# Performance work log

Measured on AMD Instinct MI355X. Metric: run time of the kernel, lower is better.

Reference implementation:

```python
import jax, jax.numpy as jnp
import numpy as np


def setup_inputs() -> dict:
    key = jax.random.key(0)
    kq, kk, kv = jax.random.split(key, 3)
    B, T, D = 8, 4096, 64
    q = jax.random.normal(kq, (B, T, D), dtype=jnp.float32)
    k = jax.random.normal(kk, (B, T, D), dtype=jnp.float32)
    v = jax.random.normal(kv, (B, T, D), dtype=jnp.float32)
    return {"q": q, "k": k, "v": v}


def reference(q, k, v):
    # q,k,v: [b, t, d]
    b, t_q, d = q.shape
    t_k = k.shape[1]
    scale = 1.0 / jnp.sqrt(jnp.asarray(d, dtype=q.dtype))
    qk = jnp.einsum('bqd,bkd->bqk', q, k) * scale  # [b, t_q, t_k]
    # causal mask: positions t2 > t1 set to -inf (replaces the Python double-loop)
    causal_mask = jnp.arange(t_k)[None, :] > jnp.arange(t_q)[:, None]  # [t_q, t_k]
    qk = jnp.where(causal_mask[None, :, :], -jnp.inf, qk)
    attn = jax.nn.softmax(qk, axis=-1)
    return jnp.einsum('bqk,bkd->bqd', attn, v)
```

## Files before the change

### kernel.cpp

```cpp
#include <hip/hip_runtime.h>

namespace {

constexpr float QSC = 0.18033688f;

typedef short bf16x8 __attribute__((ext_vector_type(8)));
typedef float f32x4 __attribute__((ext_vector_type(4)));

typedef __attribute__((address_space(3))) unsigned int lds_u32;
typedef __attribute__((address_space(1))) const unsigned int gbl_u32;

__device__ inline float exp2x(float x) { return __builtin_amdgcn_exp2f(x); }

__device__ inline unsigned int pack2(float a, float b) {
  unsigned int ua = __builtin_bit_cast(unsigned int, a);
  unsigned int ub = __builtin_bit_cast(unsigned int, b);
  ua = (ua + 0x8000u) >> 16;
  ub = (ub + 0x8000u) & 0xFFFF0000u;
  return ua | ub;
}

__device__ inline void gl_lds16(const unsigned short* g, unsigned short* l) {
  __builtin_amdgcn_global_load_lds((gbl_u32*)g, (lds_u32*)l, 16, 0, 0);
}

__device__ inline bf16x8 ld16(const unsigned short* p) {
  uint4 u = *(const uint4*)p;
  return __builtin_bit_cast(bf16x8, u);
}

__global__ __launch_bounds__(256) void prep(const float* __restrict__ K,
                                            const float* __restrict__ V,
                                            unsigned short* __restrict__ Kbf,
                                            unsigned short* __restrict__ Vtb) {
  __shared__ float Vl[64 * 65];
  const int bid = blockIdx.x;
  const int b = bid >> 6, kt = bid & 63;
  const int tid = threadIdx.x;
  const float4* Ks4 = (const float4*)(K + ((size_t)b * 4096 + kt * 64) * 64);
  const float4* Vs4 = (const float4*)(V + ((size_t)b * 4096 + kt * 64) * 64);
  #pragma unroll
  for (int i = 0; i < 4; ++i) {
    int idx = tid + 256 * i;
    int row = idx >> 4, c4 = idx & 15;
    float4 t = Ks4[idx];
    *(uint2*)&Kbf[((size_t)b * 4096 + kt * 64 + row) * 64 + c4 * 4] =
        make_uint2(pack2(t.x, t.y), pack2(t.z, t.w));
    float4 tv = Vs4[idx];
    float* d = &Vl[row * 65 + c4 * 4];
    d[0] = tv.x; d[1] = tv.y; d[2] = tv.z; d[3] = tv.w;
  }
  __syncthreads();
  #pragma unroll
  for (int i = 0; i < 4; ++i) {
    int idx = tid + 256 * i;
    int dd = idx >> 4, kc = idx & 15;
    float a  = Vl[(kc * 4 + 0) * 65 + dd];
    float b2 = Vl[(kc * 4 + 1) * 65 + dd];
    float c  = Vl[(kc * 4 + 2) * 65 + dd];
    float e  = Vl[(kc * 4 + 3) * 65 + dd];
    *(uint2*)&Vtb[((size_t)b * 64 + dd) * 4096 + kt * 64 + kc * 4] =
        make_uint2(pack2(a, b2), pack2(c, e));
  }
}

__launch_bounds__(512, 4)
__global__ void fa_mfma(const float* __restrict__ Q,
                        float* __restrict__ O,
                        const unsigned short* __restrict__ Kbf,
                        const unsigned short* __restrict__ Vtb) {
  __shared__ __align__(16) unsigned short smem[32768];

  const int bid = blockIdx.x;
  int b, qt;
  if (bid < 256) { b = bid & 7; qt = bid >> 3; }
  else           { b = bid & 7; qt = 63 - ((bid - 256) >> 3); }

  const int tid  = threadIdx.x;
  const int w    = tid >> 6;
  const int g    = w >> 2;
  const int wg   = w & 3;
  const int lane = tid & 63;
  const int quad = lane >> 4;
  const int lc   = lane & 15;

  unsigned short* Kb0 = &smem[(g * 2 + 0) * 4096];
  unsigned short* Kb1 = &smem[(g * 2 + 1) * 4096];
  unsigned short* Vb  = &smem[16384 + g * 4096];
  unsigned short* Pl  = &smem[24576 + w * 1024];

  const unsigned short* Kt_g = Kbf + (size_t)b * 4096 * 64;
  const unsigned short* Vt_g = Vtb + (size_t)b * 64 * 4096;

  const int r0 = wg * 16 + (lane >> 3);
  const int c0 = (lane & 7) ^ (r0 & 7);

  const int ph0 = (quad ^ (lc & 7)) * 8;
  const int ph1 = ((4 + quad) ^ (lc & 7)) * 8;

  const size_t base = (size_t)b * 4096 * 64;
  const float* Qb = Q + base + (size_t)qt * 64 * 64;
  float* Ob = O + base + (size_t)qt * 64 * 64;

  bf16x8 qf[2];
  {
    const float* qrow = Qb + (wg * 16 + lc) * 64 + quad * 8;
    #pragma unroll
    for (int ks = 0; ks < 2; ++ks) {
      float4 x = *(const float4*)(qrow + ks * 32);
      float4 y = *(const float4*)(qrow + ks * 32 + 4);
      uint4 u = make_uint4(pack2(x.x * QSC, x.y * QSC), pack2(x.z * QSC, x.w * QSC),
                           pack2(y.x * QSC, y.y * QSC), pack2(y.z * QSC, y.w * QSC));
      qf[ks] = __builtin_bit_cast(bf16x8, u);
    }
  }

  if (g <= qt) {
    const unsigned short* gk = Kt_g + (size_t)(g * 64) * 64;
    gl_lds16(gk + (size_t)r0 * 64 + c0 * 8, Kb0 + wg * 1024);
    gl_lds16(gk + (size_t)(r0 + 8) * 64 + c0 * 8, Kb0 + wg * 1024 + 512);
  }

  float l_i = 0.0f;
  f32x4 o[4];
  #pragma unroll
  for (int nt = 0; nt < 4; ++nt) o[nt] = f32x4{0.f, 0.f, 0.f, 0.f};

  const int nIter = qt / 2 + 1;
  for (int i = 0; i < nIter; ++i) {
    const int kt = 2 * i + g;
    const bool active = (kt <= qt);
    unsigned short* Kcur = (i & 1) ? Kb1 : Kb0;
    unsigned short* Knxt = (i & 1) ? Kb0 : Kb1;

    __syncthreads();

    if (active) {
      const unsigned short* gv = Vt_g + kt * 64;
      gl_lds16(gv + (size_t)r0 * 4096 + c0 * 8, Vb + wg * 1024);
      gl_lds16(gv + (size_t)(r0 + 8) * 4096 + c0 * 8, Vb + wg * 1024 + 512);
    }
    if (kt + 2 <= qt) {
      const unsigned short* gk = Kt_g + (size_t)((kt + 2) * 64) * 64;
      gl_lds16(gk + (size_t)r0 * 64 + c0 * 8, Knxt + wg * 1024);
      gl_lds16(gk + (size_t)(r0 + 8) * 64 + c0 * 8, Knxt + wg * 1024 + 512);
    }

    if (active) {
      f32x4 st[4];
      #pragma unroll
      for (int t = 0; t < 4; ++t) {
        f32x4 c = {0.f, 0.f, 0.f, 0.f};
        c = __builtin_amdgcn_mfma_f32_16x16x32_bf16(ld16(&Kcur[(t * 16 + lc) * 64 + ph0]), qf[0], c, 0, 0, 0);
        c = __builtin_amdgcn_mfma_f32_16x16x32_bf16(ld16(&Kcur[(t * 16 + lc) * 64 + ph1]), qf[1], c, 0, 0, 0);
        st[t] = c;
      }

      const bool diag = (kt == qt);
      const int qrow = wg * 16 + lc;
      #pragma unroll
      for (int t = 0; t < 4; ++t) {
        float e[4];
        #pragma unroll
        for (int r = 0; r < 4; ++r) {
          int key_l = 16 * t + quad * 4 + r;
          float v = st[t][r];
          if (diag && key_l > qrow) v = -1e30f;
          e[r] = exp2x(v);
        }
        l_i += (e[0] + e[1]) + (e[2] + e[3]);
        *(uint2*)&Pl[lc * 64 + ((2 * t + (quad >> 1)) ^ (lc & 7)) * 8 + (quad & 1) * 4] =
            make_uint2(pack2(e[0], e[1]), pack2(e[2], e[3]));
      }
    }

    __syncthreads();

    if (active) {
      #pragma unroll
      for (int ks = 0; ks < 2; ++ks) {
        bf16x8 a = ld16(&Pl[lc * 64 + (ks ? ph1 : ph0)]);
        #pragma unroll
        for (int nt = 0; nt < 4; ++nt) {
          bf16x8 bfr = ld16(&Vb[(nt * 16 + lc) * 64 + (ks ? ph1 : ph0)]);
          o[nt] = __builtin_amdgcn_mfma_f32_16x16x32_bf16(a, bfr, o[nt], 0, 0, 0);
        }
      }
    }
  }

  l_i += __shfl_xor(l_i, 16);
  l_i += __shfl_xor(l_i, 32);

  constexpr int MSTR = 66;
  float* mrg = (float*)smem;
  if (g == 1) {
    #pragma unroll
    for (int r = 0; r < 4; ++r) {
      int row = wg * 16 + quad * 4 + r;
      #pragma unroll
      for (int nt = 0; nt < 4; ++nt)
        mrg[row * MSTR + nt * 16 + lc] = o[nt][r];
    }
    if (quad == 0)
      mrg[64 * MSTR + wg * 16 + lc] = l_i;
  }
  __syncthreads();
  if (g == 0) {
    const int row0 = wg * 16 + lc;
    float linv = 1.0f / (l_i + mrg[64 * MSTR + row0]);
    float lv[4];
    #pragma unroll
    for (int r = 0; r < 4; ++r) lv[r] = __shfl(linv, quad * 4 + r);
    #pragma unroll
    for (int r = 0; r < 4; ++r) {
      int row = wg * 16 + quad * 4 + r;
      float* orow = Ob + row * 64 + lc;
      #pragma unroll
      for (int nt = 0; nt < 4; ++nt) {
        float o1 = mrg[row * MSTR + nt * 16 + lc];
        orow[nt * 16] = (o[nt][r] + o1) * lv[r];
      }
    }
  }
}

}

extern "C" void kernel_launch(void* const* d_in, const int* in_sizes, int n_in,
                              void* d_out, int out_size, void* d_ws, size_t ws_size,
                              hipStream_t stream) {
  const float* q = (const float*)d_in[0];
  const float* k = (const float*)d_in[1];
  const float* v = (const float*)d_in[2];
  float* out = (float*)d_out;
  unsigned short* Kbf = (unsigned short*)d_ws;
  unsigned short* Vtb = Kbf + (size_t)8 * 4096 * 64;
  prep<<<dim3(512), dim3(256), 0, stream>>>(k, v, Kbf, Vtb);
  fa_mfma<<<dim3(512), dim3(512), 0, stream>>>(q, out, Kbf, Vtb);
}
```

Measured before the change: 120.6 us.

## Double-buffer V, pass P through registers via permlane swaps, one barrier per iteration

V tiles are now double-buffered alongside K and prefetched one iteration ahead, so the loop needs only one barrier per step instead of two. The P matrix is rearranged into the MFMA A-operand layout in registers with v_permlane32/16_swap instead of a round trip through LDS. s_setprio is raised around the MFMA sections. The cost is more LDS space for V buffers, redundant clamped loads past the last tile, and an explicit vmcnt(0) wait before each barrier.

```diff
diff --git a/kernel.cpp b/kernel.cpp
--- a/kernel.cpp
+++ b/kernel.cpp
@@ -27,6 +27,13 @@
 __device__ inline bf16x8 ld16(const unsigned short* p) {
   uint4 u = *(const uint4*)p;
   return __builtin_bit_cast(bf16x8, u);
+}
+
+__device__ inline void pswap32(unsigned int& a, unsigned int& b) {
+  asm volatile("v_permlane32_swap_b32 %0, %1" : "+v"(a), "+v"(b));
+}
+__device__ inline void pswap16(unsigned int& a, unsigned int& b) {
+  asm volatile("v_permlane16_swap_b32 %0, %1" : "+v"(a), "+v"(b));
 }
 
 __global__ __launch_bounds__(256) void prep(const float* __restrict__ K,
@@ -86,8 +93,8 @@
 
   unsigned short* Kb0 = &smem[(g * 2 + 0) * 4096];
   unsigned short* Kb1 = &smem[(g * 2 + 1) * 4096];
-  unsigned short* Vb  = &smem[16384 + g * 4096];
-  unsigned short* Pl  = &smem[24576 + w * 1024];
+  unsigned short* Vb0 = &smem[16384 + (g * 2 + 0) * 4096];
+  unsigned short* Vb1 = &smem[16384 + (g * 2 + 1) * 4096];
 
   const unsigned short* Kt_g = Kbf + (size_t)b * 4096 * 64;
   const unsigned short* Vt_g = Vtb + (size_t)b * 64 * 4096;
@@ -101,6 +108,16 @@
   const size_t base = (size_t)b * 4096 * 64;
   const float* Qb = Q + base + (size_t)qt * 64 * 64;
   float* Ob = O + base + (size_t)qt * 64 * 64;
+
+  {
+    const int kt0 = (g <= qt) ? g : qt;
+    const unsigned short* gk = Kt_g + (size_t)(kt0 * 64) * 64;
+    gl_lds16(gk + (size_t)r0 * 64 + c0 * 8, Kb0 + wg * 1024);
+    gl_lds16(gk + (size_t)(r0 + 8) * 64 + c0 * 8, Kb0 + wg * 1024 + 512);
+    const unsigned short* gv = Vt_g + kt0 * 64;
+    gl_lds16(gv + (size_t)r0 * 4096 + c0 * 8, Vb0 + wg * 1024);
+    gl_lds16(gv + (size_t)(r0 + 8) * 4096 + c0 * 8, Vb0 + wg * 1024 + 512);
+  }
 
   bf16x8 qf[2];
   {
@@ -115,12 +132,6 @@
     }
   }
 
-  if (g <= qt) {
-    const unsigned short* gk = Kt_g + (size_t)(g * 64) * 64;
-    gl_lds16(gk + (size_t)r0 * 64 + c0 * 8, Kb0 + wg * 1024);
-    gl_lds16(gk + (size_t)(r0 + 8) * 64 + c0 * 8, Kb0 + wg * 1024 + 512);
-  }
-
   float l_i = 0.0f;
   f32x4 o[4];
   #pragma unroll
@@ -131,23 +142,26 @@
     const int kt = 2 * i + g;
     const bool active = (kt <= qt);
     unsigned short* Kcur = (i & 1) ? Kb1 : Kb0;
+    unsigned short* Vcur = (i & 1) ? Vb1 : Vb0;
     unsigned short* Knxt = (i & 1) ? Kb0 : Kb1;
-
-    __syncthreads();
-
-    if (active) {
-      const unsigned short* gv = Vt_g + kt * 64;
-      gl_lds16(gv + (size_t)r0 * 4096 + c0 * 8, Vb + wg * 1024);
-      gl_lds16(gv + (size_t)(r0 + 8) * 4096 + c0 * 8, Vb + wg * 1024 + 512);
-    }
-    if (kt + 2 <= qt) {
-      const unsigned short* gk = Kt_g + (size_t)((kt + 2) * 64) * 64;
+    unsigned short* Vnxt = (i & 1) ? Vb0 : Vb1;
+
+    asm volatile("s_waitcnt vmcnt(0)" ::: "memory");
+    __builtin_amdgcn_s_barrier();
+
+    {
+      int ktn = 2 * (i + 1) + g; if (ktn > qt) ktn = qt;
+      const unsigned short* gk = Kt_g + (size_t)(ktn * 64) * 64;
       gl_lds16(gk + (size_t)r0 * 64 + c0 * 8, Knxt + wg * 1024);
       gl_lds16(gk + (size_t)(r0 + 8) * 64 + c0 * 8, Knxt + wg * 1024 + 512);
+      const unsigned short* gv = Vt_g + ktn * 64;
+      gl_lds16(gv + (size_t)r0 * 4096 + c0 * 8, Vnxt + wg * 1024);
+      gl_lds16(gv + (size_t)(r0 + 8) * 4096 + c0 * 8, Vnxt + wg * 1024 + 512);
     }
 
     if (active) {
       f32x4 st[4];
+      __builtin_amdgcn_s_setprio(1);
       #pragma unroll
       for (int t = 0; t < 4; ++t) {
         f32x4 c = {0.f, 0.f, 0.f, 0.f};
@@ -155,9 +169,11 @@
         c = __builtin_amdgcn_mfma_f32_16x16x32_bf16(ld16(&Kcur[(t * 16 + lc) * 64 + ph1]), qf[1], c, 0, 0, 0);
         st[t] = c;
       }
+      __builtin_amdgcn_s_setprio(0);
 
       const bool diag = (kt == qt);
       const int qrow = wg * 16 + lc;
+      unsigned int pc[4][2];
       #pragma unroll
       for (int t = 0; t < 4; ++t) {
         float e[4];
@@ -169,25 +185,29 @@
           e[r] = exp2x(v);
         }
         l_i += (e[0] + e[1]) + (e[2] + e[3]);
-        *(uint2*)&Pl[lc * 64 + ((2 * t + (quad >> 1)) ^ (lc & 7)) * 8 + (quad & 1) * 4] =
-            make_uint2(pack2(e[0], e[1]), pack2(e[2], e[3]));
-      }
-    }
-
-    __syncthreads();
-
-    if (active) {
+        pc[t][0] = pack2(e[0], e[1]);
+        pc[t][1] = pack2(e[2], e[3]);
+      }
+
+      __builtin_amdgcn_s_setprio(1);
       #pragma unroll
       for (int ks = 0; ks < 2; ++ks) {
-        bf16x8 a = ld16(&Pl[lc * 64 + (ks ? ph1 : ph0)]);
+        unsigned int x0 = pc[2 * ks][0], y0 = pc[2 * ks + 1][0];
+        unsigned int x1 = pc[2 * ks][1], y1 = pc[2 * ks + 1][1];
+        pswap32(x0, y0); pswap16(x0, y0);
+        pswap32(x1, y1); pswap16(x1, y1);
+        bf16x8 a = __builtin_bit_cast(bf16x8, make_uint4(x0, x1, y0, y1));
+        const int ph = ks ? ph1 : ph0;
         #pragma unroll
         for (int nt = 0; nt < 4; ++nt) {
-          bf16x8 bfr = ld16(&Vb[(nt * 16 + lc) * 64 + (ks ? ph1 : ph0)]);
-          o[nt] = __builtin_amdgcn_mfma_f32_16x16x32_bf16(a, bfr, o[nt], 0, 0, 0);
+          o[nt] = __builtin_amdgcn_mfma_f32_16x16x32_bf16(a, ld16(&Vcur[(nt * 16 + lc) * 64 + ph]), o[nt], 0, 0, 0);
         }
       }
-    }
-  }
+      __builtin_amdgcn_s_setprio(0);
+    }
+  }
+
+  __syncthreads();
 
   l_i += __shfl_xor(l_i, 16);
   l_i += __shfl_xor(l_i, 32);
```

Measured after the change: 120.4 us. Within noise of the previous version (-0.2%).
